# Optimization experiments

Measured on AMD Instinct MI355X. Metric: run time of the kernel, lower is better.

## Reference

```python
import jax, jax.numpy as jnp
import numpy as np

S, B, D, N, DH = 2048, 2, 1024, 16, 64  # seq, batch, d_model, n_head, d_head
LN_EPS = 1e-5


def setup_inputs() -> dict:
    key = jax.random.key(0)
    ks = jax.random.split(key, 8)
    h = jax.random.normal(ks[0], (S, B, D), dtype=jnp.float32)
    Wq = jax.random.normal(ks[1], (D, N * DH), dtype=jnp.float32) * 0.02
    Wkv = jax.random.normal(ks[2], (D, 2 * N * DH), dtype=jnp.float32) * 0.02
    Wo = jax.random.normal(ks[3], (N * DH, D), dtype=jnp.float32) * 0.02
    ln_gamma = jnp.ones((D,), dtype=jnp.float32)
    ln_beta = jnp.zeros((D,), dtype=jnp.float32)
    # persistent compressive-memory state from a previous segment
    memory = jax.random.normal(ks[4], (B, N, DH, DH), dtype=jnp.float32)
    # normalization is a sum of (elu(k)+1) over ~S positions -> strictly positive, O(S)
    mem_norm = jax.random.uniform(ks[5], (B, 1, N, DH), dtype=jnp.float32) * S + 1.0
    gate_beta = jnp.ones((1,), dtype=jnp.float32) * 0.01  # beta_eps
    return {"h": h, "Wq": Wq, "Wkv": Wkv, "Wo": Wo, "ln_gamma": ln_gamma,
            "ln_beta": ln_beta, "memory": memory, "mem_norm": mem_norm,
            "gate_beta": gate_beta}


def reference(h, Wq, Wkv, Wo, ln_gamma, ln_beta, memory, mem_norm, gate_beta):
    scale = 1.0 / np.sqrt(DH).astype(np.float32)
    # projections (pre_lnorm=False, mems=None -> c == h)
    q = (h @ Wq).reshape(S, B, N, DH)
    k, v = jnp.split(h @ Wkv, 2, axis=-1)
    k = k.reshape(S, B, N, DH)
    v = v.reshape(S, B, N, DH)
    # local quadratic attention
    score = jnp.einsum('ibnd,jbnd->ijbn', q, k) * scale  # [S,S,B,N]
    prob = jax.nn.softmax(score, axis=1)
    attn_vec = jnp.einsum('ijbn,jbnd->ibnd', prob, v).reshape(S, B, N * DH)
    # memory retrieval (NOTE: source swaps K/V in the _update_memory call;
    # it is done under no_grad -> stop_gradient here)
    cached_Q = jax.nn.elu(q.swapaxes(0, 1)) + 1.0          # [B,S,N,DH]
    num = jnp.einsum('bsnk,bnkv->bsnv', cached_Q, memory)   # [B,S,N,DH]
    den = jnp.einsum('bsnk,bvnk->bsnv', cached_Q, mem_norm)  # [B,S,N,1]
    content_A = jax.lax.stop_gradient(num / den)            # [B,S,N,DH]
    # gated injection
    g = jax.nn.sigmoid(gate_beta)                           # [1]
    inj = g * content_A.swapaxes(0, 1).reshape(S, B, N * DH) + (1.0 - g) * attn_vec
    attn_out = inj @ Wo
    # post layernorm residual
    y = h + attn_out
    mu = jnp.mean(y, axis=-1, keepdims=True)
    var = jnp.mean((y - mu) ** 2, axis=-1, keepdims=True)
    return (y - mu) / jnp.sqrt(var + LN_EPS) * ln_gamma + ln_beta
```

## Files before the change

kernel.cpp:

```cpp
#include <hip/hip_runtime.h>


typedef unsigned short ushort_t;
typedef unsigned int uint32;

typedef __bf16 bf16x8 __attribute__((ext_vector_type(8)));
typedef float f32x4 __attribute__((ext_vector_type(4)));
typedef float f32x16 __attribute__((ext_vector_type(16)));
typedef unsigned short u16x8 __attribute__((ext_vector_type(8)));
typedef unsigned short u16x4 __attribute__((ext_vector_type(4)));
typedef unsigned int u32x4 __attribute__((ext_vector_type(4)));

typedef const __attribute__((address_space(1))) void gvoid_t;
typedef __attribute__((address_space(3))) void lvoid_t;

#define S_LEN 2048
#define BATCH 2
#define NHEAD 16

__device__ __forceinline__ ushort_t f2bf(float x) {
  union { float f; unsigned u; } c; c.f = x;
  unsigned r = (c.u + 0x7FFFu + ((c.u >> 16) & 1u)) >> 16;
  return (ushort_t)r;
}
__device__ __forceinline__ float bf2f(ushort_t v) {
  union { unsigned u; float f; } c; c.u = ((unsigned)v) << 16;
  return c.f;
}

__global__ __launch_bounds__(256) void k_cvt_h(const float* __restrict__ src,
                                               ushort_t* __restrict__ dst, int n4) {
  int idx = blockIdx.x * 256 + threadIdx.x;
  if (idx >= n4) return;
  float4 v = ((const float4*)src)[idx];
  u16x4 o; o[0] = f2bf(v.x); o[1] = f2bf(v.y); o[2] = f2bf(v.z); o[3] = f2bf(v.w);
  ((u16x4*)dst)[idx] = o;
}

__global__ __launch_bounds__(256) void k_cvt_wT3(const float* __restrict__ Wq,
                                                 const float* __restrict__ Wkv,
                                                 const float* __restrict__ Wo,
                                                 ushort_t* __restrict__ wT,
                                                 ushort_t* __restrict__ woT) {
  const int z = blockIdx.z;
  const float* W;
  ushort_t* WT;
  int N;
  if (z == 0)      { W = Wq;  WT = wT;                          N = 1024; }
  else if (z == 1) { W = Wkv; WT = wT + (size_t)1024 * 1024;    N = 2048; }
  else             { W = Wo;  WT = woT;                         N = 1024; }
  const int K = 1024;
  if (blockIdx.x * 32 >= N) return;
  __shared__ float tile[32][33];
  const int n0 = blockIdx.x * 32, k0 = blockIdx.y * 32;
  const int tx = threadIdx.x & 31, ty = threadIdx.x >> 5;
#pragma unroll
  for (int r = 0; r < 32; r += 8)
    tile[ty + r][tx] = W[(size_t)(k0 + ty + r) * N + n0 + tx];
  __syncthreads();
#pragma unroll
  for (int r = 0; r < 32; r += 8)
    WT[(size_t)(n0 + ty + r) * K + k0 + tx] = f2bf(tile[tx][ty + r]);
}

template <int OUT_BF16>
__global__ __launch_bounds__(256) void k_gemm_bt(const ushort_t* __restrict__ A,
                                                 const ushort_t* __restrict__ B,
                                                 void* __restrict__ Cv, int M, int N, int K,
                                                 int nbx) {
  __shared__ __attribute__((aligned(16))) ushort_t As[128 * 32];
  __shared__ __attribute__((aligned(16))) ushort_t Bs[128 * 32];
  const int per = gridDim.x >> 3;
  const int fl = (blockIdx.x & 7) * per + (blockIdx.x >> 3);
  const int m0 = (fl / nbx) * 128, n0 = (fl % nbx) * 128;
  const int tid = threadIdx.x, w = tid >> 6, lane = tid & 63;
  const int wm = (w >> 1) * 64, wn = (w & 1) * 64;
  const int l15 = lane & 15, l4 = lane >> 4;
  f32x4 acc[4][4];
#pragma unroll
  for (int i = 0; i < 4; ++i)
#pragma unroll
    for (int j = 0; j < 4; ++j)
#pragma unroll
      for (int r = 0; r < 4; ++r) acc[i][j][r] = 0.f;

  for (int k0 = 0; k0 < K; k0 += 32) {
    __syncthreads();
#pragma unroll
    for (int r = 0; r < 2; ++r) {
      int c = r * 256 + w * 64 + lane;
      const ushort_t* ga = A + (size_t)(m0 + (c >> 2)) * K + k0 + (c & 3) * 8;
      const ushort_t* gb = B + (size_t)(n0 + (c >> 2)) * K + k0 + (c & 3) * 8;
      __builtin_amdgcn_global_load_lds((gvoid_t*)ga, (lvoid_t*)(As + (r * 256 + w * 64) * 8), 16, 0, 0);
      __builtin_amdgcn_global_load_lds((gvoid_t*)gb, (lvoid_t*)(Bs + (r * 256 + w * 64) * 8), 16, 0, 0);
    }
    __syncthreads();
    bf16x8 af[4], bfr[4];
#pragma unroll
    for (int i = 0; i < 4; ++i) af[i] = *(const bf16x8*)&As[(wm + i * 16 + l15) * 32 + l4 * 8];
#pragma unroll
    for (int j = 0; j < 4; ++j) bfr[j] = *(const bf16x8*)&Bs[(wn + j * 16 + l15) * 32 + l4 * 8];
#pragma unroll
    for (int i = 0; i < 4; ++i)
#pragma unroll
      for (int j = 0; j < 4; ++j)
        acc[i][j] = __builtin_amdgcn_mfma_f32_16x16x32_bf16(af[i], bfr[j], acc[i][j], 0, 0, 0);
  }
#pragma unroll
  for (int i = 0; i < 4; ++i)
#pragma unroll
    for (int j = 0; j < 4; ++j)
#pragma unroll
      for (int r = 0; r < 4; ++r) {
        int row = m0 + wm + i * 16 + l4 * 4 + r;
        int col = n0 + wn + j * 16 + l15;
        if (OUT_BF16)
          ((ushort_t*)Cv)[(size_t)row * N + col] = f2bf(acc[i][j][r]);
        else
          ((float*)Cv)[(size_t)row * N + col] = acc[i][j][r];
      }
}

__global__ __launch_bounds__(256) void k_gemm64(const ushort_t* __restrict__ A,
                                                const ushort_t* __restrict__ B,
                                                float* __restrict__ C, int M, int N, int K,
                                                int nbx) {
  __shared__ __attribute__((aligned(16))) ushort_t As[64 * 32];
  __shared__ __attribute__((aligned(16))) ushort_t Bs[128 * 32];
  const int per = gridDim.x >> 3;
  const int fl = (blockIdx.x & 7) * per + (blockIdx.x >> 3);
  const int m0 = (fl / nbx) * 64, n0 = (fl % nbx) * 128;
  const int tid = threadIdx.x, w = tid >> 6, lane = tid & 63;
  const int wn = w * 32;
  const int l15 = lane & 15, l4 = lane >> 4;
  f32x4 acc[4][2];
#pragma unroll
  for (int i = 0; i < 4; ++i)
#pragma unroll
    for (int j = 0; j < 2; ++j)
#pragma unroll
      for (int r = 0; r < 4; ++r) acc[i][j][r] = 0.f;

  for (int k0 = 0; k0 < K; k0 += 32) {
    __syncthreads();
    {
      int c = w * 64 + lane;
      const ushort_t* ga = A + (size_t)(m0 + (c >> 2)) * K + k0 + (c & 3) * 8;
      __builtin_amdgcn_global_load_lds((gvoid_t*)ga, (lvoid_t*)(As + w * 512), 16, 0, 0);
#pragma unroll
      for (int r = 0; r < 2; ++r) {
        int c2 = r * 256 + w * 64 + lane;
        const ushort_t* gb = B + (size_t)(n0 + (c2 >> 2)) * K + k0 + (c2 & 3) * 8;
        __builtin_amdgcn_global_load_lds((gvoid_t*)gb, (lvoid_t*)(Bs + r * 2048 + w * 512), 16, 0, 0);
      }
    }
    __syncthreads();
    bf16x8 af[4], bfr[2];
#pragma unroll
    for (int i = 0; i < 4; ++i) af[i] = *(const bf16x8*)&As[(i * 16 + l15) * 32 + l4 * 8];
#pragma unroll
    for (int j = 0; j < 2; ++j) bfr[j] = *(const bf16x8*)&Bs[(wn + j * 16 + l15) * 32 + l4 * 8];
#pragma unroll
    for (int i = 0; i < 4; ++i)
#pragma unroll
      for (int j = 0; j < 2; ++j)
        acc[i][j] = __builtin_amdgcn_mfma_f32_16x16x32_bf16(af[i], bfr[j], acc[i][j], 0, 0, 0);
  }
#pragma unroll
  for (int i = 0; i < 4; ++i)
#pragma unroll
    for (int j = 0; j < 2; ++j)
#pragma unroll
      for (int r = 0; r < 4; ++r)
        C[(size_t)(m0 + i * 16 + l4 * 4 + r) * N + n0 + wn + j * 16 + l15] = acc[i][j][r];
}

__global__ __launch_bounds__(256) void k_vt(const ushort_t* __restrict__ qkv,
                                            ushort_t* __restrict__ vt) {
  __shared__ uint32 tile[64 * 65];
  const int jt = blockIdx.x, bn = blockIdx.y, b = bn & 1, n = bn >> 1;
  const int tid = threadIdx.x;
  const int j0 = jt * 64;
#pragma unroll
  for (int rr = 0; rr < 2; ++rr) {
    int lin = rr * 2048 + tid * 8;
    int j = lin >> 6, d0 = lin & 63;
    u16x8 v = *(const u16x8*)(qkv + (size_t)(j0 + j) * 6144 + b * 3072 + 2048 + n * 64 + d0);
#pragma unroll
    for (int e = 0; e < 8; ++e) tile[j * 65 + d0 + e] = v[e];
  }
  __syncthreads();
#pragma unroll
  for (int rr = 0; rr < 2; ++rr) {
    int lin = rr * 2048 + tid * 8;
    int d = lin >> 6, jj = lin & 63;
    u16x8 o;
#pragma unroll
    for (int e = 0; e < 8; ++e) o[e] = (ushort_t)tile[(jj + e) * 65 + d];
    *(u16x8*)(vt + ((size_t)bn * 64 + d) * 2048 + j0 + jj) = o;
  }
}

__device__ __forceinline__ void stage_k(const ushort_t* __restrict__ qkv, ushort_t* kw,
                                        int j0, int b, int n, int w, int lane) {
#pragma unroll
  for (int r = 0; r < 2; ++r) {
    int jb_ = w * 16 + r * 8;
    int jb8 = w * 2 + r;
    const ushort_t* ksrc = qkv + (size_t)(j0 + jb_ + (lane >> 3)) * 6144 + b * 3072 + n * 64 + 1024
                           + ((((lane & 7) ^ (lane >> 3) ^ jb8) & 7) << 3);
    __builtin_amdgcn_global_load_lds((gvoid_t*)ksrc, (lvoid_t*)(kw + jb_ * 64), 16, 0, 0);
  }
}
__device__ __forceinline__ void stage_vt(const ushort_t* __restrict__ vt, ushort_t* vw,
                                         int j0, int bn, int w, int lane) {
#pragma unroll
  for (int r = 0; r < 2; ++r) {
    int db_ = w * 16 + r * 8;
    int jb8 = w * 2 + r;
    const ushort_t* vsrc = vt + ((size_t)bn * 64 + db_ + (lane >> 3)) * 2048 + j0
                           + ((((lane & 7) ^ (lane >> 3) ^ jb8) & 7) << 3);
    __builtin_amdgcn_global_load_lds((gvoid_t*)vsrc, (lvoid_t*)(vw + db_ * 64), 16, 0, 0);
  }
}

__global__ __launch_bounds__(256) void k_attn(const ushort_t* __restrict__ qkv,
                                              const ushort_t* __restrict__ vt,
                                              const float* __restrict__ mem,
                                              const float* __restrict__ mnorm,
                                              const float* __restrict__ gbeta,
                                              ushort_t* __restrict__ inj) {
  __shared__ __attribute__((aligned(16))) ushort_t Ks[3][4096];
  __shared__ __attribute__((aligned(16))) ushort_t VTs[3][4096];
  const int bn = blockIdx.y, b = bn & 1, n = bn >> 1;
  const int tid = threadIdx.x, w = tid >> 6, lane = tid & 63;
  const int l31 = lane & 31, h = lane >> 5;
  const int qrow = blockIdx.x * 128 + w * 32 + l31;
  const size_t qoff = (size_t)qrow * 6144 + b * 3072 + n * 64;
  const float CEXP = 0.18033688011113723f;
  bf16x8 qf[4];
#pragma unroll
  for (int ks = 0; ks < 4; ++ks) {
    u16x8 qv = *(const u16x8*)(qkv + qoff + ks * 16 + h * 8);
    union { u16x8 u; bf16x8 v; } cu;
#pragma unroll
    for (int e = 0; e < 8; ++e) cu.u[e] = f2bf(bf2f(qv[e]) * CEXP);
    qf[ks] = cu.v;
  }
  const int fA = (l31 & 7) ^ (l31 >> 3);
  const int fB = fA ^ 4;
  union { u16x8 u; bf16x8 v; } ones;
#pragma unroll
  for (int e = 0; e < 8; ++e) ones.u[e] = 0x3F80;

  stage_k(qkv, Ks[0], 0, b, n, w, lane);
  stage_vt(vt, VTs[0], 0, bn, w, lane);
  stage_k(qkv, Ks[1], 64, b, n, w, lane);
  stage_vt(vt, VTs[1], 64, bn, w, lane);

  f32x16 oacc[2], lacc;
#pragma unroll
  for (int r = 0; r < 16; ++r) { oacc[0][r] = 0.f; oacc[1][r] = 0.f; lacc[r] = 0.f; }

  int cur = 0, stg = 2;
  for (int t = 0; t < 32; ++t) {
    if (t + 2 < 32) {
      stage_k(qkv, Ks[stg], (t + 2) * 64, b, n, w, lane);
      stage_vt(vt, VTs[stg], (t + 2) * 64, bn, w, lane);
    }
    if (t < 30)       asm volatile("s_waitcnt vmcnt(8)" ::: "memory");
    else if (t == 30) asm volatile("s_waitcnt vmcnt(4)" ::: "memory");
    else              asm volatile("s_waitcnt vmcnt(0)" ::: "memory");
    __builtin_amdgcn_s_barrier();

    const ushort_t* Kb = Ks[cur];
    const ushort_t* Vb = VTs[cur];
    f32x16 sv[2];
#pragma unroll
    for (int r = 0; r < 16; ++r) { sv[0][r] = 0.f; sv[1][r] = 0.f; }
    __builtin_amdgcn_s_setprio(1);
#pragma unroll
    for (int jb = 0; jb < 2; ++jb) {
      const int rb = (jb * 32 + l31) * 64;
      const int fj = jb ? fB : fA;
#pragma unroll
      for (int ks = 0; ks < 4; ++ks) {
        bf16x8 kf = *(const bf16x8*)&Kb[rb + ((((ks << 1) | h) ^ fj) << 3)];
        sv[jb] = __builtin_amdgcn_mfma_f32_32x32x16_bf16(kf, qf[ks], sv[jb], 0, 0, 0);
      }
    }
    __builtin_amdgcn_s_setprio(0);
#pragma unroll
    for (int jb = 0; jb < 2; ++jb)
#pragma unroll
      for (int r = 0; r < 16; ++r)
        sv[jb][r] = __builtin_amdgcn_exp2f(sv[jb][r]);
#pragma unroll
    for (int ks = 0; ks < 4; ++ks) {
      const int jb = ks >> 1, q0 = (ks & 1) * 2;
      uint32 X0, X1, Y0, Y1;
      asm volatile("v_cvt_pk_bf16_f32 %0, %1, %2" : "=v"(X0) : "v"(sv[jb][q0 * 4 + 0]), "v"(sv[jb][q0 * 4 + 1]));
      asm volatile("v_cvt_pk_bf16_f32 %0, %1, %2" : "=v"(X1) : "v"(sv[jb][q0 * 4 + 2]), "v"(sv[jb][q0 * 4 + 3]));
      asm volatile("v_cvt_pk_bf16_f32 %0, %1, %2" : "=v"(Y0) : "v"(sv[jb][(q0 + 1) * 4 + 0]), "v"(sv[jb][(q0 + 1) * 4 + 1]));
      asm volatile("v_cvt_pk_bf16_f32 %0, %1, %2" : "=v"(Y1) : "v"(sv[jb][(q0 + 1) * 4 + 2]), "v"(sv[jb][(q0 + 1) * 4 + 3]));
      asm volatile("v_permlane32_swap_b32 %0, %1" : "+v"(X0), "+v"(Y0));
      asm volatile("v_permlane32_swap_b32 %0, %1" : "+v"(X1), "+v"(Y1));
      union { u32x4 u; bf16x8 v; } pf;
      pf.u[0] = X0; pf.u[1] = X1; pf.u[2] = Y0; pf.u[3] = Y1;
      const int c = (ks << 1) | h;
      bf16x8 vf0 = *(const bf16x8*)&Vb[l31 * 64 + ((c ^ fA) << 3)];
      bf16x8 vf1 = *(const bf16x8*)&Vb[(32 + l31) * 64 + ((c ^ fB) << 3)];
      __builtin_amdgcn_s_setprio(1);
      oacc[0] = __builtin_amdgcn_mfma_f32_32x32x16_bf16(vf0, pf.v, oacc[0], 0, 0, 0);
      oacc[1] = __builtin_amdgcn_mfma_f32_32x32x16_bf16(vf1, pf.v, oacc[1], 0, 0, 0);
      lacc = __builtin_amdgcn_mfma_f32_32x32x16_bf16(ones.v, pf.v, lacc, 0, 0, 0);
      __builtin_amdgcn_s_setprio(0);
    }
    __builtin_amdgcn_s_barrier();
    cur = (cur + 1 == 3) ? 0 : cur + 1;
    stg = (stg + 1 == 3) ? 0 : stg + 1;
  }
  const float l_run = lacc[0];

  float den = 0.f;
  bf16x8 cqf[4];
  const float* nrm = mnorm + (size_t)(b * NHEAD + n) * 64;
#pragma unroll
  for (int ks = 0; ks < 4; ++ks) {
    u16x8 qv = *(const u16x8*)(qkv + qoff + ks * 16 + h * 8);
    union { u16x8 u; bf16x8 v; } cu;
#pragma unroll
    for (int e = 0; e < 8; ++e) {
      float x = bf2f(qv[e]);
      float c = (x > 0.f) ? (x + 1.f) : __builtin_amdgcn_exp2f(x * 1.4426950408889634f);
      cu.u[e] = f2bf(c);
      den += c * nrm[ks * 16 + h * 8 + e];
    }
    cqf[ks] = cu.v;
  }
  den += __shfl_xor(den, 32);

  const float* mb = mem + (size_t)(b * NHEAD + n) * 4096;
  f32x16 accv[2];
#pragma unroll
  for (int r = 0; r < 16; ++r) { accv[0][r] = 0.f; accv[1][r] = 0.f; }
#pragma unroll
  for (int db = 0; db < 2; ++db)
#pragma unroll
    for (int ks = 0; ks < 4; ++ks) {
      union { u16x8 u; bf16x8 v; } af;
#pragma unroll
      for (int e = 0; e < 8; ++e)
        af.u[e] = f2bf(mb[(size_t)(ks * 16 + h * 8 + e) * 64 + db * 32 + l31]);
      accv[db] = __builtin_amdgcn_mfma_f32_32x32x16_bf16(af.v, cqf[ks], accv[db], 0, 0, 0);
    }

  float g = 1.f / (1.f + expf(-gbeta[0]));
  float rden = 1.f / den, invl = 1.f / l_run;
  ushort_t* op = inj + (size_t)qrow * 2048 + b * 1024 + n * 64;
#pragma unroll
  for (int db = 0; db < 2; ++db)
#pragma unroll
    for (int qq = 0; qq < 4; ++qq) {
      u16x4 st;
#pragma unroll
      for (int m = 0; m < 4; ++m) {
        float content = accv[db][qq * 4 + m] * rden;
        float av = oacc[db][qq * 4 + m] * invl;
        st[m] = f2bf(g * content + (1.f - g) * av);
      }
      *(u16x4*)(op + db * 32 + qq * 8 + h * 4) = st;
    }
}

__global__ __launch_bounds__(256) void k_ln(const float* __restrict__ h,
                                            const float* __restrict__ ao,
                                            const float* __restrict__ gam,
                                            const float* __restrict__ bet,
                                            float* __restrict__ out) {
  const int m = blockIdx.x, t = threadIdx.x;
  const int lane = t & 63, w = t >> 6;
  __shared__ float redS[4], redQ[4];
  const size_t base = (size_t)m * 1024;
  float4 hv = ((const float4*)(h + base))[t];
  float4 avv = ((const float4*)(ao + base))[t];
  float y0 = hv.x + avv.x, y1 = hv.y + avv.y, y2 = hv.z + avv.z, y3 = hv.w + avv.w;
  float s = y0 + y1 + y2 + y3;
  float sq = y0 * y0 + y1 * y1 + y2 * y2 + y3 * y3;
#pragma unroll
  for (int mk = 32; mk >= 1; mk >>= 1) { s += __shfl_xor(s, mk); sq += __shfl_xor(sq, mk); }
  if (lane == 0) { redS[w] = s; redQ[w] = sq; }
  __syncthreads();
  float Ssum = redS[0] + redS[1] + redS[2] + redS[3];
  float Qsum = redQ[0] + redQ[1] + redQ[2] + redQ[3];
  float mu = Ssum * (1.f / 1024.f);
  float var = Qsum * (1.f / 1024.f) - mu * mu;
  float rstd = rsqrtf(var + 1e-5f);
  float4 g = ((const float4*)gam)[t];
  float4 bt = ((const float4*)bet)[t];
  float4 o;
  o.x = (y0 - mu) * rstd * g.x + bt.x;
  o.y = (y1 - mu) * rstd * g.y + bt.y;
  o.z = (y2 - mu) * rstd * g.z + bt.z;
  o.w = (y3 - mu) * rstd * g.w + bt.w;
  ((float4*)(out + base))[t] = o;
}

extern "C" void kernel_launch(void* const* d_in, const int* in_sizes, int n_in,
                              void* d_out, int out_size, void* d_ws, size_t ws_size,
                              hipStream_t stream) {
  const float* h = (const float*)d_in[0];
  const float* Wq = (const float*)d_in[1];
  const float* Wkv = (const float*)d_in[2];
  const float* Wo = (const float*)d_in[3];
  const float* gam = (const float*)d_in[4];
  const float* bet = (const float*)d_in[5];
  const float* mem = (const float*)d_in[6];
  const float* mnorm = (const float*)d_in[7];
  const float* gbeta = (const float*)d_in[8];
  float* out = (float*)d_out;

  char* ws = (char*)d_ws;
  ushort_t* hb  = (ushort_t*)(ws);
  ushort_t* wT  = (ushort_t*)(ws + (size_t)(8u << 20));
  ushort_t* woT = (ushort_t*)(ws + (size_t)(14u << 20));
  ushort_t* qkv = (ushort_t*)(ws + (size_t)(16u << 20));
  float*    ao  = (float*)   (ws + (size_t)(16u << 20));
  ushort_t* vtb = (ushort_t*)(ws + (size_t)(40u << 20));
  ushort_t* inj = hb;

  k_cvt_h<<<4096, 256, 0, stream>>>(h, hb, 1048576);
  k_cvt_wT3<<<dim3(64, 32, 3), 256, 0, stream>>>(Wq, Wkv, Wo, wT, woT);
  k_gemm_bt<1><<<768, 256, 0, stream>>>(hb, wT, (void*)qkv, 4096, 3072, 1024, 24);
  k_vt<<<dim3(32, 32), 256, 0, stream>>>(qkv, vtb);
  k_attn<<<dim3(16, 32), 256, 0, stream>>>(qkv, vtb, mem, mnorm, gbeta, inj);
  k_gemm64<<<512, 256, 0, stream>>>(inj, woT, ao, 4096, 1024, 1024, 8);
  k_ln<<<4096, 256, 0, stream>>>(h, ao, gam, bet, out);
}
```

Baseline: 145.0 us.

## Split attention keys across two blocks and move memory retrieval into a gate kernel

The attention kernel now splits the 2048 keys into two halves along a third grid dimension. Each block writes an unnormalised bf16 partial output and its row-sum: one half goes to a scratch buffer, the other into the already-consumed V slot of the qkv buffer. A new k_gate2 kernel then does the compressive-memory retrieval, sums the two partials, normalises them and applies the gate. This doubles the number of attention blocks and cuts shared memory per block to improve CU occupancy. In exchange, the 3-stage prefetch with fine-grained vmcnt waits becomes a 2-buffer scheme with full __syncthreads, and the change adds a kernel launch, extra partial-result traffic and an extra bf16 rounding of the partial outputs.

```diff
diff --git a/kernel.cpp b/kernel.cpp
--- a/kernel.cpp
+++ b/kernel.cpp
@@ -226,13 +226,12 @@
 
 __global__ __launch_bounds__(256) void k_attn(const ushort_t* __restrict__ qkv,
                                               const ushort_t* __restrict__ vt,
-                                              const float* __restrict__ mem,
-                                              const float* __restrict__ mnorm,
-                                              const float* __restrict__ gbeta,
-                                              ushort_t* __restrict__ inj) {
-  __shared__ __attribute__((aligned(16))) ushort_t Ks[3][4096];
-  __shared__ __attribute__((aligned(16))) ushort_t VTs[3][4096];
-  const int bn = blockIdx.y, b = bn & 1, n = bn >> 1;
+                                              ushort_t* o0, ushort_t* o1,
+                                              float* __restrict__ l0,
+                                              float* __restrict__ l1) {
+  __shared__ __attribute__((aligned(16))) ushort_t Ks[2][4096];
+  __shared__ __attribute__((aligned(16))) ushort_t VTs[2][4096];
+  const int bn = blockIdx.y, b = bn & 1, n = bn >> 1, z = blockIdx.z;
   const int tid = threadIdx.x, w = tid >> 6, lane = tid & 63;
   const int l31 = lane & 31, h = lane >> 5;
   const int qrow = blockIdx.x * 128 + w * 32 + l31;
@@ -253,28 +252,22 @@
 #pragma unroll
   for (int e = 0; e < 8; ++e) ones.u[e] = 0x3F80;
 
-  stage_k(qkv, Ks[0], 0, b, n, w, lane);
-  stage_vt(vt, VTs[0], 0, bn, w, lane);
-  stage_k(qkv, Ks[1], 64, b, n, w, lane);
-  stage_vt(vt, VTs[1], 64, bn, w, lane);
+  const int t0 = z * 16;
+  stage_k(qkv, Ks[0], t0 * 64, b, n, w, lane);
+  stage_vt(vt, VTs[0], t0 * 64, bn, w, lane);
+  __syncthreads();
 
   f32x16 oacc[2], lacc;
 #pragma unroll
   for (int r = 0; r < 16; ++r) { oacc[0][r] = 0.f; oacc[1][r] = 0.f; lacc[r] = 0.f; }
 
-  int cur = 0, stg = 2;
-  for (int t = 0; t < 32; ++t) {
-    if (t + 2 < 32) {
-      stage_k(qkv, Ks[stg], (t + 2) * 64, b, n, w, lane);
-      stage_vt(vt, VTs[stg], (t + 2) * 64, bn, w, lane);
-    }
-    if (t < 30)       asm volatile("s_waitcnt vmcnt(8)" ::: "memory");
-    else if (t == 30) asm volatile("s_waitcnt vmcnt(4)" ::: "memory");
-    else              asm volatile("s_waitcnt vmcnt(0)" ::: "memory");
-    __builtin_amdgcn_s_barrier();
-
-    const ushort_t* Kb = Ks[cur];
-    const ushort_t* Vb = VTs[cur];
+  for (int t = 0; t < 16; ++t) {
+    const ushort_t* Kb = Ks[t & 1];
+    const ushort_t* Vb = VTs[t & 1];
+    if (t < 15) {
+      stage_k(qkv, Ks[(t + 1) & 1], (t0 + t + 1) * 64, b, n, w, lane);
+      stage_vt(vt, VTs[(t + 1) & 1], (t0 + t + 1) * 64, bn, w, lane);
+    }
     f32x16 sv[2];
 #pragma unroll
     for (int r = 0; r < 16; ++r) { sv[0][r] = 0.f; sv[1][r] = 0.f; }
@@ -316,11 +309,39 @@
       lacc = __builtin_amdgcn_mfma_f32_32x32x16_bf16(ones.v, pf.v, lacc, 0, 0, 0);
       __builtin_amdgcn_s_setprio(0);
     }
-    __builtin_amdgcn_s_barrier();
-    cur = (cur + 1 == 3) ? 0 : cur + 1;
-    stg = (stg + 1 == 3) ? 0 : stg + 1;
-  }
-  const float l_run = lacc[0];
+    if (t < 15) __syncthreads();
+  }
+
+  ushort_t* op = (z == 0) ? (o0 + (size_t)qrow * 2048 + b * 1024 + n * 64)
+                          : (o1 + (size_t)qrow * 6144 + b * 3072 + 2048 + n * 64);
+#pragma unroll
+  for (int db = 0; db < 2; ++db)
+#pragma unroll
+    for (int qq = 0; qq < 4; ++qq) {
+      u16x4 st;
+#pragma unroll
+      for (int m = 0; m < 4; ++m) st[m] = f2bf(oacc[db][qq * 4 + m]);
+      *(u16x4*)(op + db * 32 + qq * 8 + h * 4) = st;
+    }
+  if (h == 0) {
+    float* lp = (z == 0) ? l0 : l1;
+    lp[qrow * 32 + bn] = lacc[0];
+  }
+}
+
+__global__ __launch_bounds__(256) void k_gate2(const ushort_t* __restrict__ qkv,
+                                               const ushort_t* __restrict__ o0,
+                                               const float* __restrict__ l0,
+                                               const float* __restrict__ l1,
+                                               const float* __restrict__ mem,
+                                               const float* __restrict__ mnorm,
+                                               const float* __restrict__ gbeta,
+                                               ushort_t* __restrict__ inj) {
+  const int bn = blockIdx.y, b = bn & 1, n = bn >> 1;
+  const int tid = threadIdx.x, w = tid >> 6, lane = tid & 63;
+  const int l31 = lane & 31, h = lane >> 5;
+  const int qrow = blockIdx.x * 128 + w * 32 + l31;
+  const size_t qoff = (size_t)qrow * 6144 + b * 3072 + n * 64;
 
   float den = 0.f;
   bf16x8 cqf[4];
@@ -355,21 +376,27 @@
       accv[db] = __builtin_amdgcn_mfma_f32_32x32x16_bf16(af.v, cqf[ks], accv[db], 0, 0, 0);
     }
 
+  const float lsum = l0[qrow * 32 + bn] + l1[qrow * 32 + bn];
   float g = 1.f / (1.f + expf(-gbeta[0]));
-  float rden = 1.f / den, invl = 1.f / l_run;
+  float rden = 1.f / den, invl = 1.f / lsum;
+  const ushort_t* p0 = o0 + (size_t)qrow * 2048 + b * 1024 + n * 64;
+  const ushort_t* p1 = qkv + (size_t)qrow * 6144 + b * 3072 + 2048 + n * 64;
   ushort_t* op = inj + (size_t)qrow * 2048 + b * 1024 + n * 64;
 #pragma unroll
   for (int db = 0; db < 2; ++db)
 #pragma unroll
     for (int qq = 0; qq < 4; ++qq) {
+      const int off = db * 32 + qq * 8 + h * 4;
+      u16x4 a0 = *(const u16x4*)(p0 + off);
+      u16x4 a1 = *(const u16x4*)(p1 + off);
       u16x4 st;
 #pragma unroll
       for (int m = 0; m < 4; ++m) {
+        float av = (bf2f(a0[m]) + bf2f(a1[m])) * invl;
         float content = accv[db][qq * 4 + m] * rden;
-        float av = oacc[db][qq * 4 + m] * invl;
         st[m] = f2bf(g * content + (1.f - g) * av);
       }
-      *(u16x4*)(op + db * 32 + qq * 8 + h * 4) = st;
+      *(u16x4*)(op + off) = st;
     }
 }
 
@@ -427,13 +454,17 @@
   ushort_t* qkv = (ushort_t*)(ws + (size_t)(16u << 20));
   float*    ao  = (float*)   (ws + (size_t)(16u << 20));
   ushort_t* vtb = (ushort_t*)(ws + (size_t)(40u << 20));
-  ushort_t* inj = hb;
+  ushort_t* o0  = hb;
+  float*    l0  = (float*)(ws + (size_t)(8u << 20));
+  float*    l1  = (float*)(ws + (size_t)(8u << 20) + (1u << 18));
+  ushort_t* inj = vtb;
 
   k_cvt_h<<<4096, 256, 0, stream>>>(h, hb, 1048576);
   k_cvt_wT3<<<dim3(64, 32, 3), 256, 0, stream>>>(Wq, Wkv, Wo, wT, woT);
   k_gemm_bt<1><<<768, 256, 0, stream>>>(hb, wT, (void*)qkv, 4096, 3072, 1024, 24);
   k_vt<<<dim3(32, 32), 256, 0, stream>>>(qkv, vtb);
-  k_attn<<<dim3(16, 32), 256, 0, stream>>>(qkv, vtb, mem, mnorm, gbeta, inj);
+  k_attn<<<dim3(16, 32, 2), 256, 0, stream>>>(qkv, vtb, o0, qkv, l0, l1);
+  k_gate2<<<dim3(16, 32), 256, 0, stream>>>(qkv, o0, l0, l1, mem, mnorm, gbeta, inj);
   k_gemm64<<<512, 256, 0, stream>>>(inj, woT, ao, 4096, 1024, 1024, 8);
   k_ln<<<4096, 256, 0, stream>>>(h, ao, gam, bet, out);
 }
```

New measurement: 158.5 us. +9.3%, slower.
